# Kernel optimization log

Hardware: AMD Instinct MI355X
Metric: run time of the kernel (lower is better)

The kernel has to match this reference:

```python
import jax, jax.numpy as jnp
import numpy as np

B, L, D = 2, 2048, 1024
K, M = 32, 4
H = D // K
AH = 4            # anchor heads
DH = K - AH       # decay heads
CK = 4            # conv kernel size
TOTAL = 2 * D + K + K * M


def setup_inputs() -> dict:
    key = jax.random.key(0)
    ks = jax.random.split(key, 7)
    x = jax.random.normal(ks[0], (B, L, D), jnp.float32)
    mask = jnp.ones((B, L), jnp.float32)
    W_in = jax.random.normal(ks[1], (D, TOTAL), jnp.float32) * 0.02
    conv_w = jax.random.normal(ks[2], (CK, TOTAL), jnp.float32) * 0.1  # depthwise taps
    conv_b = jnp.zeros((TOTAL,), jnp.float32)
    grid = np.linspace(-np.pi / 3, np.pi / 3, M).astype(np.float32)
    theta_base = jnp.asarray(np.tile(grid.reshape(1, 1, 1, 1, M), (1, 1, K, 1, 1)))
    theta_resid_scale = jnp.full((K,), 0.1, jnp.float32)
    dr = np.geomspace(0.001, 0.1, DH).astype(np.float32)
    decay_slopes = jnp.asarray(np.log(np.exp(dr) - 1.0).astype(np.float32))
    ar = np.geomspace(0.01, 0.1, AH).astype(np.float32)
    anchor_slopes = jnp.asarray(np.log(np.exp(ar) - 1.0).astype(np.float32))
    score_scale = jnp.ones((K,), jnp.float32)
    norm_scale = jnp.ones((2 * H * M,), jnp.float32)
    gl = float((2.0 / (H * M + H)) ** 0.5)  # glorot std
    W_re = jax.random.normal(ks[3], (H * M, H), jnp.float32) * gl
    W_im = jax.random.normal(ks[4], (H * M, H), jnp.float32) * gl
    W_out = jax.random.normal(ks[5], (D, D), jnp.float32) * 0.02
    return dict(x=x, mask=mask, W_in=W_in, conv_w=conv_w, conv_b=conv_b,
                theta_base=theta_base, theta_resid_scale=theta_resid_scale,
                decay_slopes=decay_slopes, anchor_slopes=anchor_slopes,
                score_scale=score_scale, norm_scale=norm_scale,
                W_re=W_re, W_im=W_im, W_out=W_out)


def _forward(x, mask, W_in, conv_w, conv_b, theta_base, theta_resid_scale,
             decay_slopes, anchor_slopes, score_scale, norm_scale, W_re, W_im, W_out):
    b, l, d = x.shape
    z = x @ W_in  # (b,l,TOTAL)
    # causal depthwise conv, kernel size CK
    zp = jnp.pad(z, ((0, 0), (CK - 1, 0), (0, 0)))
    z = sum(zp[:, t:t + l, :] * conv_w[t] for t in range(CK)) + conv_b

    x_val = z[..., :D].reshape(b, l, K, H)
    x_gate = jax.nn.silu(z[..., D:2 * D])
    s_raw = z[..., 2 * D:2 * D + K].reshape(b, l, K, 1)
    theta_raw = z[..., 2 * D + K:].reshape(b, l, K, M)

    theta_delta = theta_raw / (1.0 + jnp.abs(theta_raw))
    theta_dyn = theta_base + theta_resid_scale.reshape(1, 1, K, 1, 1) * (
        theta_delta.reshape(b, l, K, 1, M) * jnp.float32(np.pi / 3))

    m = mask[:, :, None, None]
    s_raw = s_raw * m
    x_val = x_val * m

    pos = jnp.arange(l, dtype=jnp.float32)
    slopes_d = jax.nn.softplus(decay_slopes).reshape(1, 1, DH, 1)
    dist_d = jnp.maximum(jnp.float32(l - 1) - pos, 0.0)[None, :, None, None]
    w_decay = jnp.exp(-slopes_d * dist_d)
    slopes_a = jax.nn.softplus(anchor_slopes).reshape(1, 1, AH, 1)
    w_anchor = jnp.exp(-slopes_a * pos[None, :, None, None])
    time_weight = jnp.concatenate([w_decay, w_anchor], axis=2)  # (1,l,K,1)

    p = jnp.exp(jnp.clip(score_scale[None, None, :, None] * s_raw, -20.0, 20.0))
    p = p * m

    phi = x_val[..., None] * theta_dyn  # (b,l,K,H,M)
    cos_b = jnp.cos(phi)
    sin_b = jnp.sin(phi)
    p_w = (p * time_weight)[..., None]  # (b,l,K,1,1)

    flat = (b, l, K * H * M)
    merged = jnp.concatenate([
        (p_w * cos_b).reshape(flat),
        (p_w * sin_b).reshape(flat),
        jnp.broadcast_to(p_w, (b, l, K, H, M)).reshape(flat)], axis=-1)
    cs = jnp.cumsum(merged, axis=1)
    num_re, num_im, den = jnp.split(cs, 3, axis=-1)
    inv_den = 1.0 / jnp.maximum(den, jnp.float32(1e-4))
    re = (num_re * inv_den).reshape(b, l, K, H * M)
    im = (num_im * inv_den).reshape(b, l, K, H * M)

    mean_sq = (jnp.sum(re * re, axis=-1) + jnp.sum(im * im, axis=-1)) * (1.0 / (2.0 * H * M))
    rsq = jax.lax.rsqrt(mean_sq[..., None] + 1e-5)
    y = (re * rsq * norm_scale[:H * M]) @ W_re + (im * rsq * norm_scale[H * M:]) @ W_im  # (b,l,K,H)
    y = y.reshape(b, l, D)
    return (y * x_gate) @ W_out


def reference(x, mask, W_in, conv_w, conv_b, theta_base, theta_resid_scale,
              decay_slopes, anchor_slopes, score_scale, norm_scale, W_re, W_im, W_out):
    return _forward(x, mask, W_in, conv_w, conv_b, theta_base, theta_resid_scale,
                    decay_slopes, anchor_slopes, score_scale, norm_scale, W_re, W_im, W_out)
```

## Files before the change

kernel.cpp:

```cpp
#include <hip/hip_runtime.h>
#include <hip/hip_bf16.h>
#include <math.h>

#define B_ 2
#define L_ 2048
#define D_ 1024
#define K_ 32
#define M_ 4
#define H_ 32
#define AH_ 4
#define DH_ 28
#define CK_ 4
#define TOTAL_ 2208
#define NPAD_ 2304
#define BL_ (B_*L_)
#define CL_ 16
#define NC_ (L_/CL_)
#define CTS_ 280

typedef __attribute__((ext_vector_type(8))) short bf16x8;
typedef __attribute__((ext_vector_type(4))) float f32x4;

static __device__ inline unsigned short f2bu(float f) {
    union { __hip_bfloat16 h; unsigned short u; } cv;
    cv.h = __float2bfloat16(f);
    return cv.u;
}
static __device__ inline float b2f(unsigned short u) {
    union { unsigned short u; __hip_bfloat16 h; } cv;
    cv.u = u;
    return __bfloat162float(cv.h);
}
static __device__ inline float conv4(float bias, const float w[4], float r0, float r1,
                                     float r2, float zc) {
    return fmaf(w[3], zc, fmaf(w[2], r2, fmaf(w[1], r1, fmaf(w[0], r0, bias))));
}

__global__ __launch_bounds__(256) void prep_all(const float* __restrict__ x,
                                                const float* __restrict__ W_in,
                                                const float* __restrict__ Wout,
                                                const float* __restrict__ Wre,
                                                const float* __restrict__ Wim,
                                                const float* __restrict__ nscale,
                                                ushort* __restrict__ x_bf,
                                                ushort* __restrict__ Wt_in,
                                                ushort* __restrict__ Wt_o,
                                                ushort* __restrict__ W2B) {
    __shared__ float tile[64][65];
    int bid = blockIdx.x, t = threadIdx.x;
    if (bid < 4096) {
        int i = bid * 256 + t;
        float4 v = ((const float4*)x)[i];
        ushort4 o;
        o.x = f2bu(v.x); o.y = f2bu(v.y); o.z = f2bu(v.z); o.w = f2bu(v.w);
        *(ushort4*)(x_bf + (size_t)i * 4) = o;
        return;
    }
    const float* src; ushort* dst; int Kd, N, n0, k0;
    if (bid < 4096 + 576) {
        int bb = bid - 4096;
        src = W_in; dst = Wt_in; Kd = 1024; N = TOTAL_;
        n0 = (bb % 36) * 64; k0 = (bb / 36) * 64;
    } else if (bid < 4096 + 576 + 256) {
        int bb = bid - 4096 - 576;
        src = Wout; dst = Wt_o; Kd = 1024; N = 1024;
        n0 = (bb % 16) * 64; k0 = (bb / 16) * 64;
    } else {
        int ch = t;
        float ns = nscale[ch];
        for (int ho = 0; ho < 32; ++ho) {
            float w = (ch < 128) ? Wre[ch * 32 + ho] : Wim[(ch - 128) * 32 + ho];
            W2B[ho * 256 + ch] = f2bu(ns * w);
        }
        return;
    }
#pragma unroll
    for (int i = 0; i < 16; ++i) {
        int idx = t + i * 256;
        int r = idx >> 6, c = idx & 63;
        int gn = n0 + c;
        tile[r][c] = (gn < N) ? src[(size_t)(k0 + r) * N + gn] : 0.f;
    }
    __syncthreads();
#pragma unroll
    for (int i = 0; i < 16; ++i) {
        int idx = t + i * 256;
        int r = idx >> 6, c = idx & 63;
        dst[(size_t)(n0 + r) * Kd + k0 + c] = f2bu(tile[c][r]);
    }
}

__global__ __launch_bounds__(256) void gemm_bt(const ushort* __restrict__ A,
                                               const ushort* __restrict__ Bt,
                                               float* __restrict__ C,
                                               int Kd, int ldc) {
    __shared__ __align__(16) ushort As[128 * 32];
    __shared__ __align__(16) ushort Bs[128 * 32];
    int tid = threadIdx.x;
    int wave = tid >> 6, lane = tid & 63;
    int quad = lane >> 4, l16 = lane & 15;
    int m0 = blockIdx.y * 128, n0 = blockIdx.x * 128;
    int wm = (wave >> 1) * 64, wn = (wave & 1) * 64;
    f32x4 acc[4][4];
#pragma unroll
    for (int i = 0; i < 4; ++i)
#pragma unroll
        for (int j = 0; j < 4; ++j) acc[i][j] = (f32x4){0.f, 0.f, 0.f, 0.f};

    int swzq = quad ^ (l16 & 3);

    for (int k0 = 0; k0 < Kd; k0 += 32) {
#pragma unroll
        for (int i = 0; i < 2; ++i) {
            int s = i * 256 + tid;
            int row = s >> 2;
            int qg = (s & 3) ^ (row & 3);
            const ushort* ga = A + (size_t)(m0 + row) * Kd + k0 + qg * 8;
            const ushort* gb = Bt + (size_t)(n0 + row) * Kd + k0 + qg * 8;
            __builtin_amdgcn_global_load_lds((const __attribute__((address_space(1))) void*)ga,
                                             (__attribute__((address_space(3))) void*)(As + (size_t)s * 8),
                                             16, 0, 0);
            __builtin_amdgcn_global_load_lds((const __attribute__((address_space(1))) void*)gb,
                                             (__attribute__((address_space(3))) void*)(Bs + (size_t)s * 8),
                                             16, 0, 0);
        }
        __syncthreads();
        bf16x8 af[4], bfr[4];
#pragma unroll
        for (int mi = 0; mi < 4; ++mi)
            af[mi] = *(const bf16x8*)(As + (size_t)(wm + mi * 16 + l16) * 32 + swzq * 8);
#pragma unroll
        for (int ni = 0; ni < 4; ++ni)
            bfr[ni] = *(const bf16x8*)(Bs + (size_t)(wn + ni * 16 + l16) * 32 + swzq * 8);
#pragma unroll
        for (int mi = 0; mi < 4; ++mi)
#pragma unroll
            for (int ni = 0; ni < 4; ++ni)
                acc[mi][ni] = __builtin_amdgcn_mfma_f32_16x16x32_bf16(af[mi], bfr[ni], acc[mi][ni], 0, 0, 0);
        __syncthreads();
    }
#pragma unroll
    for (int mi = 0; mi < 4; ++mi)
#pragma unroll
        for (int ni = 0; ni < 4; ++ni)
#pragma unroll
            for (int r = 0; r < 4; ++r) {
                int gm = m0 + wm + mi * 16 + quad * 4 + r;
                int gn = n0 + wn + ni * 16 + l16;
                C[(size_t)gm * ldc + gn] = acc[mi][ni][r];
            }
}

__global__ __launch_bounds__(128) void pass1f(const float* __restrict__ z,
                                              const float* __restrict__ mask,
                                              const float* __restrict__ theta_base,
                                              const float* __restrict__ trs_,
                                              const float* __restrict__ dslopes,
                                              const float* __restrict__ aslopes,
                                              const float* __restrict__ sscale_,
                                              const float* __restrict__ conv_w,
                                              const float* __restrict__ conv_b,
                                              const ushort* __restrict__ W2B,
                                              float* __restrict__ cs_re,
                                              float* __restrict__ cs_im,
                                              float* __restrict__ cs_den,
                                              float* __restrict__ vc,
                                              float* __restrict__ ucs) {
    __shared__ __align__(16) ushort ct[CL_ * CTS_];
    int nc = blockIdx.x, k = blockIdx.y, b = blockIdx.z;
    int hm = threadIdx.x;
    int h = hm >> 2, m = hm & 3;
    int bk = b * K_ + k;
    size_t bkL = (size_t)bk * L_;
    int cxv = k * H_ + h, csc = 2 * D_ + k, cth = 2 * D_ + K_ + k * M_ + m;
    float wx[4], ws4[4], wt4[4];
#pragma unroll
    for (int t = 0; t < 4; ++t) {
        wx[t] = conv_w[t * TOTAL_ + cxv];
        ws4[t] = conv_w[t * TOTAL_ + csc];
        wt4[t] = conv_w[t * TOTAL_ + cth];
    }
    float bx = conv_b[cxv], bs = conv_b[csc], bt = conv_b[cth];
    int l0 = nc * CL_;
    float rx[3], rs[3], rt[3];
#pragma unroll
    for (int j = 0; j < 3; ++j) {
        int ls = l0 - 3 + j;
        if (ls >= 0) {
            size_t zo = (size_t)(b * L_ + ls) * NPAD_;
            rx[j] = z[zo + cxv]; rs[j] = z[zo + csc]; rt[j] = z[zo + cth];
        } else { rx[j] = 0.f; rs[j] = 0.f; rt[j] = 0.f; }
    }
    float raw = (k < DH_) ? dslopes[k] : aslopes[k - DH_];
    float slope = log1pf(__expf(raw));
    float sscale = sscale_[k], trsv = trs_[k], tb = theta_base[k * M_ + m];
    const float PI3 = 1.04719755119659775f;
    float tw = (k < DH_) ? __expf(-slope * (float)(L_ - 1 - l0)) : __expf(-slope * (float)l0);
    float e_s = (k < DH_) ? __expf(slope) : __expf(-slope);
    float are = 0.f, aim = 0.f, aden = 0.f;
#pragma unroll 4
    for (int i = 0; i < CL_; ++i) {
        int l = l0 + i;
        int row = b * L_ + l;
        size_t zo = (size_t)row * NPAD_;
        float zx = z[zo + cxv], zs = z[zo + csc], zt = z[zo + cth];
        float mval = mask[row];
        float xv = conv4(bx, wx, rx[0], rx[1], rx[2], zx) * mval;
        float s_raw = conv4(bs, ws4, rs[0], rs[1], rs[2], zs) * mval;
        float tr = conv4(bt, wt4, rt[0], rt[1], rt[2], zt);
        rx[0] = rx[1]; rx[1] = rx[2]; rx[2] = zx;
        rs[0] = rs[1]; rs[1] = rs[2]; rs[2] = zs;
        rt[0] = rt[1]; rt[1] = rt[2]; rt[2] = zt;
        float arg = fminf(fmaxf(sscale * s_raw, -20.f), 20.f);
        float p = __expf(arg) * mval;
        float pw = p * tw;
        tw *= e_s;
        float td = tr / (1.f + fabsf(tr));
        float theta = tb + trsv * (td * PI3);
        float phi = xv * theta;
        float sv = __sinf(phi), cv = __cosf(phi);
        unsigned short cu_re = f2bu(pw * cv);
        unsigned short cu_im = f2bu(pw * sv);
        are += b2f(cu_re); aim += b2f(cu_im); aden += pw;
        ct[i * CTS_ + hm] = cu_re;
        ct[i * CTS_ + 128 + hm] = cu_im;
    }
    size_t o = ((size_t)(bk * NC_ + nc)) * 128 + hm;
    cs_re[o] = are;
    cs_im[o] = aim;
    if (hm == 0) cs_den[bk * NC_ + nc] = aden;
    __syncthreads();
    int wave = hm >> 6, lane = hm & 63;
    int quad = lane >> 4, l16 = lane & 15;
    f32x4 acc = (f32x4){0.f, 0.f, 0.f, 0.f};
#pragma unroll
    for (int ks = 0; ks < 8; ++ks) {
        bf16x8 af = *(const bf16x8*)(ct + (size_t)l16 * CTS_ + ks * 32 + quad * 8);
        bf16x8 bfr = *(const bf16x8*)(W2B + (size_t)(wave * 16 + l16) * 256 + ks * 32 + quad * 8);
        acc = __builtin_amdgcn_mfma_f32_16x16x32_bf16(af, bfr, acc, 0, 0, 0);
    }
    size_t vbase = (bkL + l0) * 32;
#pragma unroll
    for (int r = 0; r < 4; ++r) {
        int rowv = quad * 4 + r;
        vc[vbase + (size_t)rowv * 32 + wave * 16 + l16] = acc[r];
    }
    float part = acc[0] + acc[1] + acc[2] + acc[3];
    part += __shfl_xor(part, 16, 64);
    part += __shfl_xor(part, 32, 64);
    if (quad == 0) ucs[((size_t)(bk * NC_ + nc)) * 32 + wave * 16 + l16] = part;
}

__global__ void scan2(float* cs_re, float* cs_im, float* cs_den,
                      const float* __restrict__ ucs, float* __restrict__ u_prev) {
    int bid = blockIdx.x, tid = threadIdx.x;
    if (bid < 65) {
        int seq = bid * 256 + tid;
        if (seq >= B_ * K_ * 257) return;
        int bk = seq / 257;
        int ch = seq % 257;
        float* base;
        int stride;
        if (ch < 128) { base = cs_re + (size_t)bk * NC_ * 128 + ch; stride = 128; }
        else if (ch < 256) { base = cs_im + (size_t)bk * NC_ * 128 + (ch - 128); stride = 128; }
        else { base = cs_den + (size_t)bk * NC_; stride = 1; }
        float run = 0.f;
#pragma unroll 4
        for (int i = 0; i < NC_; ++i) {
            float v = base[(size_t)i * stride];
            base[(size_t)i * stride] = run;
            run += v;
        }
    } else {
        int idx = (bid - 65) * 256 + tid;
        int hout = idx & 31;
        int bk = idx >> 5;
        float run = 0.f;
#pragma unroll 8
        for (int nc = 0; nc < NC_; ++nc) {
            size_t o = ((size_t)bk * NC_ + nc) * 32 + hout;
            float v = ucs[o];
            u_prev[o] = run;
            run += v;
        }
    }
}

__global__ __launch_bounds__(64) void scan_k7(const float* __restrict__ z,
                                              const float* __restrict__ mask,
                                              const float* __restrict__ theta_base,
                                              const float* __restrict__ trs_,
                                              const float* __restrict__ dslopes,
                                              const float* __restrict__ aslopes,
                                              const float* __restrict__ sscale_,
                                              const float* __restrict__ conv_w,
                                              const float* __restrict__ conv_b,
                                              const float* __restrict__ cs_re,
                                              const float* __restrict__ cs_im,
                                              const float* __restrict__ cs_den,
                                              const float* __restrict__ u_prev,
                                              const float* __restrict__ vc,
                                              ushort* __restrict__ gq) {
    int nc = blockIdx.x, k = blockIdx.y, b = blockIdx.z;
    int lane = threadIdx.x;
    int bk = b * K_ + k;
    size_t bkL = (size_t)bk * L_;
    int h0 = lane >> 2, m = lane & 3;
    int hout = lane & 31;
    int c0 = k * H_ + h0, c1 = k * H_ + 16 + h0;
    int csc = 2 * D_ + k, cth = 2 * D_ + K_ + k * M_ + m, cg = D_ + k * H_ + hout;
    float w0[4], w1[4], ws4[4], wt4[4], wg[4];
#pragma unroll
    for (int t = 0; t < 4; ++t) {
        w0[t] = conv_w[t * TOTAL_ + c0];
        w1[t] = conv_w[t * TOTAL_ + c1];
        ws4[t] = conv_w[t * TOTAL_ + csc];
        wt4[t] = conv_w[t * TOTAL_ + cth];
        wg[t] = conv_w[t * TOTAL_ + cg];
    }
    float b0c = conv_b[c0], b1c = conv_b[c1], bsc = conv_b[csc], btc = conv_b[cth], bgc = conv_b[cg];
    int l0 = nc * CL_;
    float r0[3], r1[3], rs[3], rt[3], rg[3];
#pragma unroll
    for (int j = 0; j < 3; ++j) {
        int ls = l0 - 3 + j;
        if (ls >= 0) {
            size_t zo = (size_t)(b * L_ + ls) * NPAD_;
            r0[j] = z[zo + c0]; r1[j] = z[zo + c1]; rs[j] = z[zo + csc];
            rt[j] = z[zo + cth]; rg[j] = z[zo + cg];
        } else { r0[j] = 0.f; r1[j] = 0.f; rs[j] = 0.f; rt[j] = 0.f; rg[j] = 0.f; }
    }
    float raw = (k < DH_) ? dslopes[k] : aslopes[k - DH_];
    float slope = log1pf(__expf(raw));
    float sscale = sscale_[k], trsv = trs_[k], tb = theta_base[k * M_ + m];
    const float PI3 = 1.04719755119659775f;
    float tw = (k < DH_) ? __expf(-slope * (float)(L_ - 1 - l0)) : __expf(-slope * (float)l0);
    float e_s = (k < DH_) ? __expf(slope) : __expf(-slope);

    size_t o = ((size_t)(bk * NC_ + nc)) * 128;
    float are0 = cs_re[o + lane];
    float are1 = cs_re[o + 64 + lane];
    float aim0 = cs_im[o + lane];
    float aim1 = cs_im[o + 64 + lane];
    float den = cs_den[bk * NC_ + nc];
    float u = u_prev[((size_t)(bk * NC_ + nc)) * 32 + hout];

#pragma unroll 4
    for (int i = 0; i < CL_; ++i) {
        int l = l0 + i;
        int row = b * L_ + l;
        size_t zo = (size_t)row * NPAD_;
        float z0 = z[zo + c0], z1 = z[zo + c1], zs = z[zo + csc];
        float zt = z[zo + cth], zg = z[zo + cg];
        float mval = mask[row];
        float xv0 = conv4(b0c, w0, r0[0], r0[1], r0[2], z0) * mval;
        float xv1 = conv4(b1c, w1, r1[0], r1[1], r1[2], z1) * mval;
        float s_raw = conv4(bsc, ws4, rs[0], rs[1], rs[2], zs) * mval;
        float tr = conv4(btc, wt4, rt[0], rt[1], rt[2], zt);
        float gpre = conv4(bgc, wg, rg[0], rg[1], rg[2], zg);
        r0[0] = r0[1]; r0[1] = r0[2]; r0[2] = z0;
        r1[0] = r1[1]; r1[1] = r1[2]; r1[2] = z1;
        rs[0] = rs[1]; rs[1] = rs[2]; rs[2] = zs;
        rt[0] = rt[1]; rt[1] = rt[2]; rt[2] = zt;
        rg[0] = rg[1]; rg[1] = rg[2]; rg[2] = zg;
        float arg = fminf(fmaxf(sscale * s_raw, -20.f), 20.f);
        float p = __expf(arg) * mval;
        float pw = p * tw;
        tw *= e_s;
        float td = tr / (1.f + fabsf(tr));
        float theta = tb + trsv * (td * PI3);
        float s0 = __sinf(xv0 * theta), cv0 = __cosf(xv0 * theta);
        float s1 = __sinf(xv1 * theta), cv1 = __cosf(xv1 * theta);
        float cre0 = b2f(f2bu(pw * cv0)), cim0 = b2f(f2bu(pw * s0));
        float cre1 = b2f(f2bu(pw * cv1)), cim1 = b2f(f2bu(pw * s1));
        are0 += cre0; aim0 += cim0; are1 += cre1; aim1 += cim1;
        den += pw;
        float s = are0 * are0 + are1 * are1 + aim0 * aim0 + aim1 * aim1;
#pragma unroll
        for (int off = 32; off; off >>= 1) s += __shfl_xor(s, off, 64);
        float inv = 1.f / fmaxf(den, 1e-4f);
        float rsq = rsqrtf(inv * inv * s * (1.0f / 256.0f) + 1e-5f);
        float scv = inv * rsq;
        u += vc[(bkL + l) * 32 + hout];
        float y = scv * u;
        float gate = gpre / (1.f + __expf(-gpre));
        if (lane < 32) gq[(size_t)row * D_ + k * H_ + hout] = f2bu(y * gate);
    }
}

extern "C" void kernel_launch(void* const* d_in, const int* in_sizes, int n_in,
                              void* d_out, int out_size, void* d_ws, size_t ws_size,
                              hipStream_t stream) {
    const float* x = (const float*)d_in[0];
    const float* mask = (const float*)d_in[1];
    const float* W_in = (const float*)d_in[2];
    const float* conv_w = (const float*)d_in[3];
    const float* conv_b = (const float*)d_in[4];
    const float* theta_base = (const float*)d_in[5];
    const float* trs = (const float*)d_in[6];
    const float* dsl = (const float*)d_in[7];
    const float* asl = (const float*)d_in[8];
    const float* ssc = (const float*)d_in[9];
    const float* nsc = (const float*)d_in[10];
    const float* Wre = (const float*)d_in[11];
    const float* Wim = (const float*)d_in[12];
    const float* Wout = (const float*)d_in[13];
    float* out = (float*)d_out;

    char* ws = (char*)d_ws;
    float* z      = (float*)(ws);
    ushort* x_bf  = (ushort*)(ws + 37748736ULL);
    ushort* Wt_in = (ushort*)(ws + 46137344ULL);
    ushort* Wt_o  = (ushort*)(ws + 50855936ULL);
    ushort* W2B   = (ushort*)(ws + 52953088ULL);
    float* vc     = (float*)(ws + 52969472ULL);
    float* cs_re  = (float*)(ws + 69746688ULL);
    float* cs_im  = (float*)(ws + 73940992ULL);
    float* cs_den = (float*)(ws + 78135296ULL);
    float* ucs    = (float*)(ws + 78168064ULL);
    float* u_prev = (float*)(ws + 79216640ULL);
    ushort* gq    = (ushort*)(ws + 80265216ULL);

    prep_all<<<4096 + 576 + 256 + 1, 256, 0, stream>>>(x, W_in, Wout, Wre, Wim, nsc,
                                                       x_bf, Wt_in, Wt_o, W2B);
    gemm_bt<<<dim3(NPAD_ / 128, BL_ / 128), 256, 0, stream>>>(x_bf, Wt_in, z, 1024, NPAD_);
    pass1f<<<dim3(NC_, K_, B_), 128, 0, stream>>>(z, mask, theta_base, trs, dsl, asl, ssc,
                                                  conv_w, conv_b, W2B,
                                                  cs_re, cs_im, cs_den, vc, ucs);
    scan2<<<73, 256, 0, stream>>>(cs_re, cs_im, cs_den, ucs, u_prev);
    scan_k7<<<dim3(NC_, K_, B_), 64, 0, stream>>>(z, mask, theta_base, trs, dsl, asl, ssc,
                                                  conv_w, conv_b, cs_re, cs_im, cs_den,
                                                  u_prev, vc, gq);
    gemm_bt<<<dim3(D_ / 128, BL_ / 128), 256, 0, stream>>>(gq, Wt_o, out, 1024, 1024);
}
```

Measured before the change: 260.0 us.

## Store projected activations in bf16 and use 64x128 GEMM tiles

```diff
diff --git a/kernel.cpp b/kernel.cpp
--- a/kernel.cpp
+++ b/kernel.cpp
@@ -90,20 +90,20 @@
     }
 }
 
-__global__ __launch_bounds__(256) void gemm_bt(const ushort* __restrict__ A,
-                                               const ushort* __restrict__ Bt,
-                                               float* __restrict__ C,
-                                               int Kd, int ldc) {
-    __shared__ __align__(16) ushort As[128 * 32];
-    __shared__ __align__(16) ushort Bs[128 * 32];
+template <bool OUT_BF16>
+__global__ __launch_bounds__(256) void gemm_bt64(const ushort* __restrict__ A,
+                                                 const ushort* __restrict__ Bt,
+                                                 void* __restrict__ Cv,
+                                                 int Kd, int ldc) {
+    __shared__ __align__(16) ushort SB[192 * 32];
     int tid = threadIdx.x;
     int wave = tid >> 6, lane = tid & 63;
     int quad = lane >> 4, l16 = lane & 15;
-    int m0 = blockIdx.y * 128, n0 = blockIdx.x * 128;
-    int wm = (wave >> 1) * 64, wn = (wave & 1) * 64;
-    f32x4 acc[4][4];
-#pragma unroll
-    for (int i = 0; i < 4; ++i)
+    int n0 = blockIdx.x * 128, m0 = blockIdx.y * 64;
+    int wm = (wave & 1) * 32, wn = (wave >> 1) * 64;
+    f32x4 acc[2][4];
+#pragma unroll
+    for (int i = 0; i < 2; ++i)
 #pragma unroll
         for (int j = 0; j < 4; ++j) acc[i][j] = (f32x4){0.f, 0.f, 0.f, 0.f};
 
@@ -111,47 +111,47 @@
 
     for (int k0 = 0; k0 < Kd; k0 += 32) {
 #pragma unroll
-        for (int i = 0; i < 2; ++i) {
+        for (int i = 0; i < 3; ++i) {
             int s = i * 256 + tid;
             int row = s >> 2;
             int qg = (s & 3) ^ (row & 3);
-            const ushort* ga = A + (size_t)(m0 + row) * Kd + k0 + qg * 8;
-            const ushort* gb = Bt + (size_t)(n0 + row) * Kd + k0 + qg * 8;
-            __builtin_amdgcn_global_load_lds((const __attribute__((address_space(1))) void*)ga,
-                                             (__attribute__((address_space(3))) void*)(As + (size_t)s * 8),
-                                             16, 0, 0);
-            __builtin_amdgcn_global_load_lds((const __attribute__((address_space(1))) void*)gb,
-                                             (__attribute__((address_space(3))) void*)(Bs + (size_t)s * 8),
+            const ushort* g = (row < 64) ? A + (size_t)(m0 + row) * Kd + k0 + qg * 8
+                                         : Bt + (size_t)(n0 + row - 64) * Kd + k0 + qg * 8;
+            __builtin_amdgcn_global_load_lds((const __attribute__((address_space(1))) void*)g,
+                                             (__attribute__((address_space(3))) void*)(SB + (size_t)s * 8),
                                              16, 0, 0);
         }
         __syncthreads();
-        bf16x8 af[4], bfr[4];
-#pragma unroll
-        for (int mi = 0; mi < 4; ++mi)
-            af[mi] = *(const bf16x8*)(As + (size_t)(wm + mi * 16 + l16) * 32 + swzq * 8);
+        bf16x8 af[2], bfr[4];
+#pragma unroll
+        for (int mi = 0; mi < 2; ++mi)
+            af[mi] = *(const bf16x8*)(SB + (size_t)(wm + mi * 16 + l16) * 32 + swzq * 8);
 #pragma unroll
         for (int ni = 0; ni < 4; ++ni)
-            bfr[ni] = *(const bf16x8*)(Bs + (size_t)(wn + ni * 16 + l16) * 32 + swzq * 8);
-#pragma unroll
-        for (int mi = 0; mi < 4; ++mi)
+            bfr[ni] = *(const bf16x8*)(SB + (size_t)(64 + wn + ni * 16 + l16) * 32 + swzq * 8);
+#pragma unroll
+        for (int mi = 0; mi < 2; ++mi)
 #pragma unroll
             for (int ni = 0; ni < 4; ++ni)
                 acc[mi][ni] = __builtin_amdgcn_mfma_f32_16x16x32_bf16(af[mi], bfr[ni], acc[mi][ni], 0, 0, 0);
         __syncthreads();
     }
 #pragma unroll
-    for (int mi = 0; mi < 4; ++mi)
+    for (int mi = 0; mi < 2; ++mi)
 #pragma unroll
         for (int ni = 0; ni < 4; ++ni)
 #pragma unroll
             for (int r = 0; r < 4; ++r) {
                 int gm = m0 + wm + mi * 16 + quad * 4 + r;
                 int gn = n0 + wn + ni * 16 + l16;
-                C[(size_t)gm * ldc + gn] = acc[mi][ni][r];
+                if (OUT_BF16)
+                    ((ushort*)Cv)[(size_t)gm * ldc + gn] = f2bu(acc[mi][ni][r]);
+                else
+                    ((float*)Cv)[(size_t)gm * ldc + gn] = acc[mi][ni][r];
             }
 }
 
-__global__ __launch_bounds__(128) void pass1f(const float* __restrict__ z,
+__global__ __launch_bounds__(128) void pass1f(const ushort* __restrict__ z,
                                               const float* __restrict__ mask,
                                               const float* __restrict__ theta_base,
                                               const float* __restrict__ trs_,
@@ -188,7 +188,7 @@
         int ls = l0 - 3 + j;
         if (ls >= 0) {
             size_t zo = (size_t)(b * L_ + ls) * NPAD_;
-            rx[j] = z[zo + cxv]; rs[j] = z[zo + csc]; rt[j] = z[zo + cth];
+            rx[j] = b2f(z[zo + cxv]); rs[j] = b2f(z[zo + csc]); rt[j] = b2f(z[zo + cth]);
         } else { rx[j] = 0.f; rs[j] = 0.f; rt[j] = 0.f; }
     }
     float raw = (k < DH_) ? dslopes[k] : aslopes[k - DH_];
@@ -203,7 +203,7 @@
         int l = l0 + i;
         int row = b * L_ + l;
         size_t zo = (size_t)row * NPAD_;
-        float zx = z[zo + cxv], zs = z[zo + csc], zt = z[zo + cth];
+        float zx = b2f(z[zo + cxv]), zs = b2f(z[zo + csc]), zt = b2f(z[zo + cth]);
         float mval = mask[row];
         float xv = conv4(bx, wx, rx[0], rx[1], rx[2], zx) * mval;
         float s_raw = conv4(bs, ws4, rs[0], rs[1], rs[2], zs) * mval;
@@ -286,7 +286,7 @@
     }
 }
 
-__global__ __launch_bounds__(64) void scan_k7(const float* __restrict__ z,
+__global__ __launch_bounds__(64) void scan_k7(const ushort* __restrict__ z,
                                               const float* __restrict__ mask,
                                               const float* __restrict__ theta_base,
                                               const float* __restrict__ trs_,
@@ -326,8 +326,8 @@
         int ls = l0 - 3 + j;
         if (ls >= 0) {
             size_t zo = (size_t)(b * L_ + ls) * NPAD_;
-            r0[j] = z[zo + c0]; r1[j] = z[zo + c1]; rs[j] = z[zo + csc];
-            rt[j] = z[zo + cth]; rg[j] = z[zo + cg];
+            r0[j] = b2f(z[zo + c0]); r1[j] = b2f(z[zo + c1]); rs[j] = b2f(z[zo + csc]);
+            rt[j] = b2f(z[zo + cth]); rg[j] = b2f(z[zo + cg]);
         } else { r0[j] = 0.f; r1[j] = 0.f; rs[j] = 0.f; rt[j] = 0.f; rg[j] = 0.f; }
     }
     float raw = (k < DH_) ? dslopes[k] : aslopes[k - DH_];
@@ -350,8 +350,8 @@
         int l = l0 + i;
         int row = b * L_ + l;
         size_t zo = (size_t)row * NPAD_;
-        float z0 = z[zo + c0], z1 = z[zo + c1], zs = z[zo + csc];
-        float zt = z[zo + cth], zg = z[zo + cg];
+        float z0 = b2f(z[zo + c0]), z1 = b2f(z[zo + c1]), zs = b2f(z[zo + csc]);
+        float zt = b2f(z[zo + cth]), zg = b2f(z[zo + cg]);
         float mval = mask[row];
         float xv0 = conv4(b0c, w0, r0[0], r0[1], r0[2], z0) * mval;
         float xv1 = conv4(b1c, w1, r1[0], r1[1], r1[2], z1) * mval;
@@ -408,22 +408,22 @@
     float* out = (float*)d_out;
 
     char* ws = (char*)d_ws;
-    float* z      = (float*)(ws);
-    ushort* x_bf  = (ushort*)(ws + 37748736ULL);
-    ushort* Wt_in = (ushort*)(ws + 46137344ULL);
-    ushort* Wt_o  = (ushort*)(ws + 50855936ULL);
-    ushort* W2B   = (ushort*)(ws + 52953088ULL);
-    float* vc     = (float*)(ws + 52969472ULL);
-    float* cs_re  = (float*)(ws + 69746688ULL);
-    float* cs_im  = (float*)(ws + 73940992ULL);
-    float* cs_den = (float*)(ws + 78135296ULL);
-    float* ucs    = (float*)(ws + 78168064ULL);
-    float* u_prev = (float*)(ws + 79216640ULL);
-    ushort* gq    = (ushort*)(ws + 80265216ULL);
+    ushort* z     = (ushort*)(ws);
+    ushort* x_bf  = (ushort*)(ws + 18874368ULL);
+    ushort* Wt_in = (ushort*)(ws + 27262976ULL);
+    ushort* Wt_o  = (ushort*)(ws + 31981568ULL);
+    ushort* W2B   = (ushort*)(ws + 34078720ULL);
+    float* vc     = (float*)(ws + 34095104ULL);
+    float* cs_re  = (float*)(ws + 50872320ULL);
+    float* cs_im  = (float*)(ws + 55066624ULL);
+    float* cs_den = (float*)(ws + 59260928ULL);
+    float* ucs    = (float*)(ws + 59293696ULL);
+    float* u_prev = (float*)(ws + 60342272ULL);
+    ushort* gq    = (ushort*)(ws + 61390848ULL);
 
     prep_all<<<4096 + 576 + 256 + 1, 256, 0, stream>>>(x, W_in, Wout, Wre, Wim, nsc,
                                                        x_bf, Wt_in, Wt_o, W2B);
-    gemm_bt<<<dim3(NPAD_ / 128, BL_ / 128), 256, 0, stream>>>(x_bf, Wt_in, z, 1024, NPAD_);
+    gemm_bt64<true><<<dim3(NPAD_ / 128, BL_ / 64), 256, 0, stream>>>(x_bf, Wt_in, z, 1024, NPAD_);
     pass1f<<<dim3(NC_, K_, B_), 128, 0, stream>>>(z, mask, theta_base, trs, dsl, asl, ssc,
                                                   conv_w, conv_b, W2B,
                                                   cs_re, cs_im, cs_den, vc, ucs);
@@ -431,5 +431,5 @@
     scan_k7<<<dim3(NC_, K_, B_), 64, 0, stream>>>(z, mask, theta_base, trs, dsl, asl, ssc,
                                                   conv_w, conv_b, cs_re, cs_im, cs_den,
                                                   u_prev, vc, gq);
-    gemm_bt<<<dim3(D_ / 128, BL_ / 128), 256, 0, stream>>>(gq, Wt_o, out, 1024, 1024);
-}
+    gemm_bt64<false><<<dim3(1024 / 128, BL_ / 64), 256, 0, stream>>>(gq, Wt_o, out, 1024, 1024);
+}
```

Measured after the change: 256.9 us. No clear change (-1.2%).
